# Kernel tuning notes

Hardware: AMD Instinct MI355X
Metric: run time of the kernel (lower is better)

The kernel has to match this reference:

```python
import jax, jax.numpy as jnp
import numpy as np

TOP_K = 30
NUM_RBF = 16
MAXREL = 32


def _normalize(x, eps=1e-12):
    return x / jnp.maximum(jnp.linalg.norm(x, axis=-1, keepdims=True), eps)


def gather_edges(edges, idx):
    # edges [B,L,L,C], idx [B,L,K] -> [B,L,K,C]
    return jnp.take_along_axis(edges, idx[..., None], axis=2)


def gather_nodes(nodes, idx):
    # nodes [B,L,C], idx [B,L,K] -> [B,L,K,C]
    B, L, K = idx.shape
    flat = idx.reshape(B, L * K)
    g = jnp.take_along_axis(nodes, flat[:, :, None], axis=1)
    return g.reshape(B, L, K, nodes.shape[-1])


def _rbf(D):
    mu = jnp.linspace(2.0, 22.0, NUM_RBF)
    sigma = (22.0 - 2.0) / NUM_RBF
    return jnp.exp(-(((D[..., None] - mu) / sigma) ** 2))


def _get_rbf(A, B, E_idx):
    D = jnp.sqrt(jnp.sum((A[:, :, None, :] - B[:, None, :, :]) ** 2, -1) + 1e-6)
    Dn = gather_edges(D[..., None], E_idx)[..., 0]
    return _rbf(Dn)


def _dist(X, mask, eps=1e-6):
    mask2 = mask[:, None, :] * mask[:, :, None]
    dX = X[:, None, :, :] - X[:, :, None, :]
    D = mask2 * jnp.sqrt(jnp.sum(dX ** 2, -1) + eps)
    D_max = jnp.max(D, -1, keepdims=True)
    D_adjust = D + (1.0 - mask2) * D_max
    k = min(TOP_K, X.shape[1])
    neg_vals, E_idx = jax.lax.top_k(-D_adjust, k)  # smallest-k distances
    D_neighbors = -neg_vals
    mask_neighbors = gather_edges(mask2[..., None], E_idx)
    return D_neighbors, E_idx, mask_neighbors


def _quaternions(R):
    # R [B,L,K,3,3] -> Q [B,L,K,4]
    diag = jnp.diagonal(R, axis1=-2, axis2=-1)
    Rxx, Ryy, Rzz = diag[..., 0], diag[..., 1], diag[..., 2]
    magnitudes = 0.5 * jnp.sqrt(jnp.abs(1.0 + jnp.stack(
        [Rxx - Ryy - Rzz, -Rxx + Ryy - Rzz, -Rxx - Ryy + Rzz], -1)))
    signs = jnp.sign(jnp.stack([
        R[..., 2, 1] - R[..., 1, 2],
        R[..., 0, 2] - R[..., 2, 0],
        R[..., 1, 0] - R[..., 0, 1]], -1))
    xyz = signs * magnitudes
    w = jnp.sqrt(jax.nn.relu(1.0 + jnp.sum(diag, -1, keepdims=True))) / 2.0
    Q = jnp.concatenate((xyz, w), -1)
    return _normalize(Q)


def _orientations_coarse(X, E_idx, eps=1e-6):
    dX = X[:, 1:, :] - X[:, :-1, :]
    dX_norm = jnp.linalg.norm(dX, axis=-1)
    dX_mask = ((dX_norm > 3.6) & (dX_norm < 4.0)).astype(X.dtype)
    dX = dX * dX_mask[:, :, None]
    U = _normalize(dX)
    u_2, u_1, u_0 = U[:, :-2, :], U[:, 1:-1, :], U[:, 2:, :]
    n_2 = _normalize(jnp.cross(u_2, u_1))
    n_1 = _normalize(jnp.cross(u_1, u_0))
    cosA = jnp.clip(-(u_1 * u_0).sum(-1), -1 + eps, 1 - eps)
    A = jnp.arccos(cosA)
    cosD = jnp.clip((n_2 * n_1).sum(-1), -1 + eps, 1 - eps)
    Dang = jnp.sign((u_2 * n_1).sum(-1)) * jnp.arccos(cosD)
    AD = jnp.stack((jnp.cos(A), jnp.sin(A) * jnp.cos(Dang),
                    jnp.sin(A) * jnp.sin(Dang)), -1)
    AD = jnp.pad(AD, ((0, 0), (1, 2), (0, 0)))  # [B,L,3]
    o_1 = _normalize(u_2 - u_1)
    O = jnp.stack((o_1, n_2, jnp.cross(o_1, n_2)), -2)  # [B,L-3,3,3]
    O = O.reshape(O.shape[0], O.shape[1], 9)
    O = jnp.pad(O, ((0, 0), (1, 2), (0, 0)))  # [B,L,9]
    O_nb = gather_nodes(O, E_idx).reshape(E_idx.shape[0], E_idx.shape[1], E_idx.shape[2], 3, 3)
    X_nb = gather_nodes(X, E_idx)
    Om = O.reshape(O.shape[0], O.shape[1], 3, 3)
    dXn = X_nb - X[:, :, None, :]
    dU = _normalize(jnp.einsum('blij,blkj->blki', Om, dXn))
    R = jnp.einsum('blji,blkjm->blkim', Om, O_nb)  # O^T @ O_neighbors
    Q = _quaternions(R)
    return AD, jnp.concatenate((dU, Q), -1)  # [B,L,3], [B,L,K,7]


def _forward(Ca, mask, residue_idx, chain_labels, pos_W, pos_b, edge_W, ln_g, ln_b):
    D_neighbors, E_idx, mask_neighbors = _dist(Ca, mask)
    Ca_0 = jnp.pad(Ca[:, :-1, :], ((0, 0), (1, 0), (0, 0)))
    Ca_1 = Ca
    Ca_2 = jnp.pad(Ca[:, 1:, :], ((0, 0), (0, 1), (0, 0)))
    V, O_features = _orientations_coarse(Ca, E_idx)
    RBF_all = jnp.concatenate([
        _rbf(D_neighbors),
        _get_rbf(Ca_0, Ca_0, E_idx),
        _get_rbf(Ca_2, Ca_2, E_idx),
        _get_rbf(Ca_0, Ca_1, E_idx),
        _get_rbf(Ca_0, Ca_2, E_idx),
        _get_rbf(Ca_1, Ca_0, E_idx),
        _get_rbf(Ca_1, Ca_2, E_idx),
        _get_rbf(Ca_2, Ca_0, E_idx),
        _get_rbf(Ca_2, Ca_1, E_idx)], -1)  # [B,L,K,144]
    offset = residue_idx[:, :, None] - residue_idx[:, None, :]
    offset = gather_edges(offset[..., None], E_idx)[..., 0]
    d_chains = (chain_labels[:, :, None] - chain_labels[:, None, :] == 0).astype(jnp.int32)
    E_chains = gather_edges(d_chains[..., None], E_idx)[..., 0]
    d = jnp.clip(offset + MAXREL, 0, 2 * MAXREL) * E_chains + (1 - E_chains) * (2 * MAXREL + 1)
    d_onehot = jax.nn.one_hot(d, 2 * MAXREL + 2, dtype=pos_W.dtype)
    E_positional = d_onehot @ pos_W + pos_b
    E = jnp.concatenate((E_positional, RBF_all, O_features), -1)  # [B,L,K,167]
    E = E @ edge_W  # no bias
    mu = jnp.mean(E, -1, keepdims=True)
    var = jnp.var(E, -1, keepdims=True)
    E = (E - mu) / jnp.sqrt(var + 1e-5) * ln_g + ln_b
    return E, E_idx


def setup_inputs() -> dict:
    key = jax.random.key(0)
    k1, k2, k3 = jax.random.split(key, 3)
    B, L = 2, 4096
    Ca = jax.random.normal(k1, (B, L, 3), dtype=jnp.float32) * 10.0
    mask = jnp.ones((B, L), dtype=jnp.float32)
    residue_idx = jnp.arange(B * L, dtype=jnp.int32).reshape(B, L) % L
    chain_labels = jnp.zeros((B, L), dtype=jnp.int32)
    pos_W = jax.random.normal(k2, (2 * MAXREL + 2, 16), dtype=jnp.float32) * 0.1
    pos_b = jnp.zeros((16,), dtype=jnp.float32)
    edge_in = 16 + NUM_RBF * 9 + 7  # 167
    edge_W = jax.random.normal(k3, (edge_in, 128), dtype=jnp.float32) * 0.05
    ln_g = jnp.ones((128,), dtype=jnp.float32)
    ln_b = jnp.zeros((128,), dtype=jnp.float32)
    return {"Ca": Ca, "mask": mask, "residue_idx": residue_idx,
            "chain_labels": chain_labels, "pos_W": pos_W, "pos_b": pos_b,
            "edge_W": edge_W, "ln_g": ln_g, "ln_b": ln_b}


def reference(Ca, mask, residue_idx, chain_labels, pos_W, pos_b, edge_W, ln_g, ln_b):
    return _forward(Ca, mask, residue_idx, chain_labels, pos_W, pos_b, edge_W, ln_g, ln_b)
```

## Files before the change

kernel.cpp:

```cpp
#include <hip/hip_runtime.h>
#include <math.h>

constexpr int Lc   = 4096;
constexpr int Bc   = 2;
constexpr int KNB  = 30;
constexpr int NF   = 167;
constexpr int NC   = 128;
constexpr int KP   = 200;
constexpr int NKT  = 6;
constexpr int CAP  = 512;

typedef __attribute__((ext_vector_type(8))) short bf16x8;
typedef __attribute__((ext_vector_type(4))) float f32x4;

struct V3 { float x, y, z; };

__device__ __forceinline__ float sgnf(float v) {
    return (v > 0.f) ? 1.f : ((v < 0.f) ? -1.f : 0.f);
}
__device__ __forceinline__ unsigned long long umin64(unsigned long long a, unsigned long long b) {
    return a < b ? a : b;
}
__device__ __forceinline__ void splitbf(float v, unsigned short& h, unsigned short& l) {
    unsigned u = __float_as_uint(v);
    h = (unsigned short)(u >> 16);
    float fh = __uint_as_float((unsigned)h << 16);
    l = (unsigned short)(__float_as_uint(v - fh) >> 16);
}
__device__ __forceinline__ unsigned cvtpk(float a, float b) {
    unsigned r;
    asm("v_cvt_pk_bf16_f32 %0, %1, %2" : "=v"(r) : "v"(a), "v"(b));
    return r;
}

__device__ __forceinline__ V3 unit_seg(float dx, float dy, float dz) {
    float n = sqrtf(dx * dx + dy * dy + dz * dz);
    float m = (n > 3.6f && n < 4.0f) ? 1.f : 0.f;
    float nn = fmaxf(m * n, 1e-12f);
    V3 r; r.x = dx * m / nn; r.y = dy * m / nn; r.z = dz * m / nn;
    return r;
}

__global__ __launch_bounds__(256) void topk_prep_kernel(
    const float* __restrict__ Ca, const float* __restrict__ mask,
    float* __restrict__ EidxF, int* __restrict__ EidxI,
    float* __restrict__ O, const float* __restrict__ W,
    unsigned short* __restrict__ Wh, unsigned short* __restrict__ Wl,
    int rows) {
    const int t = threadIdx.x;

    if (blockIdx.x >= rows) {
        int pb = blockIdx.x - rows;
        if (pb < 32) {
            int idx = pb * 256 + t;
            if (idx >= Bc * Lc) return;
            int b = idx >> 12, l = idx & (Lc - 1);
            float* o = O + (size_t)idx * 9;
            if (l < 1 || l >= Lc - 2) {
#pragma unroll
                for (int q = 0; q < 9; ++q) o[q] = 0.f;
                return;
            }
            const float* C = Ca + ((size_t)b * Lc + (l - 1)) * 3;
            V3 u2 = unit_seg(C[3] - C[0], C[4] - C[1], C[5] - C[2]);
            V3 u1 = unit_seg(C[6] - C[3], C[7] - C[4], C[8] - C[5]);
            float nx = u2.y * u1.z - u2.z * u1.y;
            float ny = u2.z * u1.x - u2.x * u1.z;
            float nz = u2.x * u1.y - u2.y * u1.x;
            float nn = fmaxf(sqrtf(nx * nx + ny * ny + nz * nz), 1e-12f);
            nx /= nn; ny /= nn; nz /= nn;
            float ox = u2.x - u1.x, oy = u2.y - u1.y, oz = u2.z - u1.z;
            float on = fmaxf(sqrtf(ox * ox + oy * oy + oz * oz), 1e-12f);
            ox /= on; oy /= on; oz /= on;
            o[0] = ox; o[1] = oy; o[2] = oz;
            o[3] = nx; o[4] = ny; o[5] = nz;
            o[6] = oy * nz - oz * ny;
            o[7] = oz * nx - ox * nz;
            o[8] = ox * ny - oy * nx;
        } else {
            int tt = (pb - 32) * 256 + t;
            if (tt >= NKT * 8 * 64) return;
            int lane = tt & 63, nt = (tt >> 6) & 7, kt = tt >> 9;
            int n = nt * 16 + (lane & 15);
            int kbase = kt * 32 + (lane >> 4) * 8;
            __align__(16) unsigned short h[8], l[8];
#pragma unroll
            for (int j = 0; j < 8; ++j) {
                int k = kbase + j;
                float v = (k < NF) ? W[(size_t)k * NC + n] : 0.f;
                splitbf(v, h[j], l[j]);
            }
            size_t o = (size_t)tt * 8;
            *(bf16x8*)(Wh + o) = *(const bf16x8*)h;
            *(bf16x8*)(Wl + o) = *(const bf16x8*)l;
        }
        return;
    }

    const int row = blockIdx.x;
    const int b = row >> 12, i = row & (Lc - 1);
    const float* CaB = Ca + (size_t)b * Lc * 3;
    const float* mB  = mask + (size_t)b * Lc;
    const float xi = CaB[i * 3 + 0], yi = CaB[i * 3 + 1], zi = CaB[i * 3 + 2];
    const float mi = mB[i];

    __shared__ unsigned long long cand[CAP];
    __shared__ float redf[4];
    __shared__ int redi[2][4];
    __shared__ int candN;

    const int lane = t & 63, wid = t >> 6;
    if (t == 0) candN = 0;

    const int j0 = t * 16;
    const float4* Ca4 = (const float4*)(CaB + (size_t)j0 * 3);
    const float4* M4  = (const float4*)(mB + j0);

    float ss[16], m2a[16];
    float lmax = -1e30f;
#pragma unroll
    for (int u = 0; u < 4; ++u) {
        float4 c0 = Ca4[u * 3 + 0];
        float4 c1 = Ca4[u * 3 + 1];
        float4 c2 = Ca4[u * 3 + 2];
        float4 mm = M4[u];
        float px[4] = {c0.x, c0.w, c1.z, c2.y};
        float py[4] = {c0.y, c1.x, c1.w, c2.z};
        float pz[4] = {c0.z, c1.y, c2.x, c2.w};
        float pm[4] = {mm.x, mm.y, mm.z, mm.w};
#pragma unroll
        for (int q = 0; q < 4; ++q) {
            float dx = px[q] - xi, dy = py[q] - yi, dz = pz[q] - zi;
            float s = dx * dx + dy * dy + dz * dz;
            float m2 = mi * pm[q];
            float v = m2 * s;
            ss[u * 4 + q] = v; m2a[u * 4 + q] = m2;
            lmax = fmaxf(lmax, v);
        }
    }
    for (int off = 32; off; off >>= 1) lmax = fmaxf(lmax, __shfl_xor(lmax, off));
    if (lane == 0) redf[wid] = lmax;
    __syncthreads();
    const float ssmax = fmaxf(fmaxf(redf[0], redf[1]), fmaxf(redf[2], redf[3]));

#pragma unroll
    for (int k = 0; k < 16; ++k) ss[k] = ss[k] + (1.f - m2a[k]) * ssmax;

    float T = ssmax * 0.037772f;
    int c = 0;
    for (int iter = 0; iter < 32; ++iter) {
        int lc = 0;
#pragma unroll
        for (int k = 0; k < 16; ++k) lc += (ss[k] <= T) ? 1 : 0;
        for (int off = 32; off; off >>= 1) lc += __shfl_xor(lc, off);
        if (lane == 0) redi[iter & 1][wid] = lc;
        __syncthreads();
        c = redi[iter & 1][0] + redi[iter & 1][1] + redi[iter & 1][2] + redi[iter & 1][3];
        if (c >= KNB && c <= 64) break;
        if (iter >= 12 && c >= KNB && c <= CAP) break;
        if (c < KNB) {
            if (c == 0) T *= 2.89f;
            else {
                float f = cbrtf((float)(KNB + 15) / (float)c);
                T *= fminf(2.89f, 1.1025f * f * f);
            }
        } else {
            float f = cbrtf(45.f / (float)c);
            T *= fmaxf(0.3025f, 1.1025f * f * f);
        }
    }

#pragma unroll
    for (int k = 0; k < 16; ++k) {
        if (ss[k] <= T) {
            int idx = atomicAdd(&candN, 1);
            if (idx < CAP)
                cand[idx] = ((unsigned long long)__float_as_uint(ss[k]) << 32) |
                            (unsigned)(j0 + k);
        }
    }
    __syncthreads();

    if (wid == 0) {
        int C = candN; if (C > CAP) C = CAP;
        if (C <= 64) {
            unsigned long long key = (lane < C) ? cand[lane] : ~0ULL;
#pragma unroll
            for (int size = 2; size <= 64; size <<= 1) {
#pragma unroll
                for (int stride = size >> 1; stride; stride >>= 1) {
                    unsigned long long other = __shfl_xor(key, stride);
                    bool dirUp = ((lane & size) == 0);
                    bool takeMin = ((lane & stride) == 0) ? dirUp : !dirUp;
                    bool less = other < key;
                    unsigned long long mn = less ? other : key;
                    unsigned long long mx = less ? key : other;
                    key = takeMin ? mn : mx;
                }
            }
            if (lane < KNB) {
                int jw = (int)(key & 0xFFFFFFFFULL);
                EidxF[(size_t)row * KNB + lane] = (float)jw;
                EidxI[(size_t)row * KNB + lane] = jw;
            }
        } else {
            unsigned long long r[CAP / 64];
#pragma unroll
            for (int q = 0; q < CAP / 64; ++q) {
                int idx = lane + q * 64;
                r[q] = (idx < C) ? cand[idx] : ~0ULL;
            }
            for (int p = 0; p < KNB; ++p) {
                unsigned long long mn = r[0];
#pragma unroll
                for (int q = 1; q < CAP / 64; ++q) mn = umin64(mn, r[q]);
                for (int off = 32; off; off >>= 1) mn = umin64(mn, __shfl_xor(mn, off));
                if (lane == 0) {
                    int jw = (int)(mn & 0xFFFFFFFFULL);
                    EidxF[(size_t)row * KNB + p] = (float)jw;
                    EidxI[(size_t)row * KNB + p] = jw;
                }
#pragma unroll
                for (int q = 0; q < CAP / 64; ++q) if (r[q] == mn) r[q] = ~0ULL;
            }
        }
    }
}

__global__ __launch_bounds__(256) void edge_kernel(
    const float* __restrict__ Ca, const int* __restrict__ ridx,
    const int* __restrict__ clab, const float* __restrict__ pos_W,
    const float* __restrict__ pos_b,
    const unsigned short* __restrict__ Wh, const unsigned short* __restrict__ Wl,
    const float* __restrict__ ln_g, const float* __restrict__ ln_b,
    const int* __restrict__ EidxI, const float* __restrict__ Omat,
    float* __restrict__ outE) {
    const int row = blockIdx.x;
    const int b = row >> 12, i = row & (Lc - 1);
    const int tid = threadIdx.x, lane = tid & 63, w = tid >> 6;

    __shared__ __align__(16) unsigned short Fh[32][KP];
    __shared__ float Ssum[32][4];
    __shared__ float Ssq[32][4];
    __shared__ float2 Mstat[32];
    __shared__ int Ej[32];

    const float* CaB = Ca + (size_t)b * Lc * 3;

    for (int q = tid; q < 32 * 33; q += 256) {
        int r = q / 33, c = 167 + q % 33;
        Fh[r][c] = 0;
    }
    for (int q = tid; q < 2 * 167; q += 256) {
        int r = 30 + q / 167, c = q % 167;
        Fh[r][c] = 0;
    }
    if (tid < KNB) Ej[tid] = EidxI[(size_t)row * KNB + tid];
    __syncthreads();

    auto putF2 = [&](int e, int k, float va, float vb) {
        *(unsigned*)&Fh[e][k] = cvtpk(va, vb);
    };
    auto loadC = [&](int n) {
        V3 r;
        if (n >= 0 && n < Lc) { r.x = CaB[n*3]; r.y = CaB[n*3+1]; r.z = CaB[n*3+2]; }
        else { r.x = 0.f; r.y = 0.f; r.z = 0.f; }
        return r;
    };

    auto rbf_task = [&](int r) {
        int e = r % 30, g = r / 30 + 1;
        int j = Ej[e];
        int pa = (int)((0xA5084u >> (2 * g)) & 3u);
        int pb = (int)((0x48984u >> (2 * g)) & 3u);
        V3 A = loadC(i - 1 + pa);
        V3 B = loadC(j - 1 + pb);
        float dx = A.x - B.x, dy = A.y - B.y, dz = A.z - B.z;
        float D8 = sqrtf(dx * dx + dy * dy + dz * dz + 1e-6f) * (1.f / 1.25f);
        int k0 = 16 * g;
#pragma unroll
        for (int m = 0; m < 16; m += 2) {
            float z0 = D8 - (2.f + (20.f / 15.f) * (float)m) * (1.f / 1.25f);
            float z1 = D8 - (2.f + (20.f / 15.f) * (float)(m + 1)) * (1.f / 1.25f);
            putF2(e, k0 + m, __expf(-z0 * z0), __expf(-z1 * z1));
        }
    };

    rbf_task(tid);

    if (w == 0) {
        if (lane < 14) rbf_task(256 + lane);
    } else if (w == 1) {
        if (lane < KNB) {
            int e = lane, j = Ej[e];
            int off = ridx[(size_t)b * Lc + i] - ridx[(size_t)b * Lc + j];
            int ec = (clab[(size_t)b * Lc + i] == clab[(size_t)b * Lc + j]) ? 1 : 0;
            int d = ec ? min(max(off + 32, 0), 64) : 65;
#pragma unroll
            for (int cc = 0; cc < 16; cc += 2)
                putF2(e, cc, pos_W[d * 16 + cc] + pos_b[cc],
                             pos_W[d * 16 + cc + 1] + pos_b[cc + 1]);
        }
    } else if (w == 2) {
        if (lane < KNB) {
            int e = lane, j = Ej[e];
            const float* Om = Omat + (size_t)row * 9;
            const float* On = Omat + ((size_t)b * Lc + j) * 9;
            V3 Ai = loadC(i), Bj = loadC(j);
            float dvx = Bj.x - Ai.x, dvy = Bj.y - Ai.y, dvz = Bj.z - Ai.z;
            float u0 = Om[0] * dvx + Om[1] * dvy + Om[2] * dvz;
            float u1 = Om[3] * dvx + Om[4] * dvy + Om[5] * dvz;
            float u2 = Om[6] * dvx + Om[7] * dvy + Om[8] * dvz;
            float un = fmaxf(sqrtf(u0 * u0 + u1 * u1 + u2 * u2), 1e-12f);
            float R[3][3];
#pragma unroll
            for (int a = 0; a < 3; ++a)
#pragma unroll
                for (int m = 0; m < 3; ++m)
                    R[a][m] = Om[0 * 3 + a] * On[0 * 3 + m] +
                              Om[1 * 3 + a] * On[1 * 3 + m] +
                              Om[2 * 3 + a] * On[2 * 3 + m];
            float Rxx = R[0][0], Ryy = R[1][1], Rzz = R[2][2];
            float m0 = 0.5f * sqrtf(fabsf(1.f + Rxx - Ryy - Rzz));
            float m1 = 0.5f * sqrtf(fabsf(1.f - Rxx + Ryy - Rzz));
            float m2 = 0.5f * sqrtf(fabsf(1.f - Rxx - Ryy + Rzz));
            float qx = sgnf(R[2][1] - R[1][2]) * m0;
            float qy = sgnf(R[0][2] - R[2][0]) * m1;
            float qz = sgnf(R[1][0] - R[0][1]) * m2;
            float qw = sqrtf(fmaxf(0.f, 1.f + Rxx + Ryy + Rzz)) * 0.5f;
            float qn = fmaxf(sqrtf(qx * qx + qy * qy + qz * qz + qw * qw), 1e-12f);
            putF2(e, 160, u0 / un, u1 / un);
            putF2(e, 162, u2 / un, qx / qn);
            putF2(e, 164, qy / qn, qz / qn);
            putF2(e, 166, qw / qn, 0.f);
        }
    }
    __syncthreads();

    const int arow = lane & 15, agrp = lane >> 4;
    const int ng0 = w * 2;
    f32x4 acc[2][2];
#pragma unroll
    for (int m = 0; m < 2; ++m)
#pragma unroll
        for (int n = 0; n < 2; ++n) acc[m][n] = (f32x4){0.f, 0.f, 0.f, 0.f};

    const bf16x8* WhF = (const bf16x8*)Wh;
    const bf16x8* WlF = (const bf16x8*)Wl;

#pragma unroll
    for (int kt = 0; kt < NKT; ++kt) {
        const int kof = kt * 32 + agrp * 8;
        bf16x8 a0 = *(const bf16x8*)&Fh[arow][kof];
        bf16x8 a1 = *(const bf16x8*)&Fh[16 + arow][kof];
        bf16x8 b0h = WhF[(kt * 8 + ng0) * 64 + lane];
        bf16x8 b1h = WhF[(kt * 8 + ng0 + 1) * 64 + lane];
        bf16x8 b0l = WlF[(kt * 8 + ng0) * 64 + lane];
        bf16x8 b1l = WlF[(kt * 8 + ng0 + 1) * 64 + lane];

        acc[0][0] = __builtin_amdgcn_mfma_f32_16x16x32_bf16(a0, b0h, acc[0][0], 0, 0, 0);
        acc[0][0] = __builtin_amdgcn_mfma_f32_16x16x32_bf16(a0, b0l, acc[0][0], 0, 0, 0);
        acc[0][1] = __builtin_amdgcn_mfma_f32_16x16x32_bf16(a0, b1h, acc[0][1], 0, 0, 0);
        acc[0][1] = __builtin_amdgcn_mfma_f32_16x16x32_bf16(a0, b1l, acc[0][1], 0, 0, 0);
        acc[1][0] = __builtin_amdgcn_mfma_f32_16x16x32_bf16(a1, b0h, acc[1][0], 0, 0, 0);
        acc[1][0] = __builtin_amdgcn_mfma_f32_16x16x32_bf16(a1, b0l, acc[1][0], 0, 0, 0);
        acc[1][1] = __builtin_amdgcn_mfma_f32_16x16x32_bf16(a1, b1h, acc[1][1], 0, 0, 0);
        acc[1][1] = __builtin_amdgcn_mfma_f32_16x16x32_bf16(a1, b1l, acc[1][1], 0, 0, 0);
    }

    float ps[2][4], pq[2][4];
#pragma unroll
    for (int m = 0; m < 2; ++m)
#pragma unroll
        for (int r = 0; r < 4; ++r) {
            float v0 = acc[m][0][r], v1 = acc[m][1][r];
            ps[m][r] = v0 + v1;
            pq[m][r] = v0 * v0 + v1 * v1;
        }
#pragma unroll
    for (int off = 1; off < 16; off <<= 1) {
#pragma unroll
        for (int m = 0; m < 2; ++m)
#pragma unroll
            for (int r = 0; r < 4; ++r) {
                ps[m][r] += __shfl_xor(ps[m][r], off);
                pq[m][r] += __shfl_xor(pq[m][r], off);
            }
    }
    if (arow == 0) {
#pragma unroll
        for (int m = 0; m < 2; ++m)
#pragma unroll
            for (int r = 0; r < 4; ++r) {
                int me = m * 16 + agrp * 4 + r;
                Ssum[me][w] = ps[m][r];
                Ssq[me][w] = pq[m][r];
            }
    }
    __syncthreads();
    if (tid < 32) {
        float s = Ssum[tid][0] + Ssum[tid][1] + Ssum[tid][2] + Ssum[tid][3];
        float q = Ssq[tid][0] + Ssq[tid][1] + Ssq[tid][2] + Ssq[tid][3];
        float mean = s * (1.f / 128.f);
        float var = q * (1.f / 128.f) - mean * mean;
        Mstat[tid] = make_float2(mean, 1.f / sqrtf(var + 1e-5f));
    }
    __syncthreads();

    float gg[2], bb[2];
#pragma unroll
    for (int n = 0; n < 2; ++n) {
        int ce = (ng0 + n) * 16 + arow;
        gg[n] = ln_g[ce];
        bb[n] = ln_b[ce];
    }
#pragma unroll
    for (int m = 0; m < 2; ++m)
#pragma unroll
        for (int r = 0; r < 4; ++r) {
            int me = m * 16 + agrp * 4 + r;
            if (me >= KNB) continue;
            float2 st = Mstat[me];
            size_t base = ((size_t)row * KNB + me) * NC;
#pragma unroll
            for (int n = 0; n < 2; ++n) {
                int ce = (ng0 + n) * 16 + arow;
                outE[base + ce] = (acc[m][n][r] - st.x) * st.y * gg[n] + bb[n];
            }
        }
}

extern "C" void kernel_launch(void* const* d_in, const int* in_sizes, int n_in,
                              void* d_out, int out_size, void* d_ws, size_t ws_size,
                              hipStream_t stream) {
    const float* Ca     = (const float*)d_in[0];
    const float* mask   = (const float*)d_in[1];
    const int*   ridx   = (const int*)d_in[2];
    const int*   clab   = (const int*)d_in[3];
    const float* pos_W  = (const float*)d_in[4];
    const float* pos_b  = (const float*)d_in[5];
    const float* edge_W = (const float*)d_in[6];
    const float* ln_g   = (const float*)d_in[7];
    const float* ln_b   = (const float*)d_in[8];

    float* outE  = (float*)d_out;
    float* EidxF = outE + (size_t)Bc * Lc * KNB * NC;

    float* Omat  = (float*)d_ws;
    int*   EidxI = (int*)(Omat + (size_t)Bc * Lc * 9);
    unsigned short* Wh = (unsigned short*)(EidxI + (size_t)Bc * Lc * KNB);
    unsigned short* Wl = Wh + (size_t)NKT * 8 * 64 * 8;

    const int rows = Bc * Lc;
    topk_prep_kernel<<<rows + 44, 256, 0, stream>>>(Ca, mask, EidxF, EidxI,
                                                    Omat, edge_W, Wh, Wl, rows);
    edge_kernel<<<rows, 256, 0, stream>>>(Ca, ridx, clab, pos_W, pos_b, Wh, Wl,
                                          ln_g, ln_b, EidxI, Omat, outE);
}
```

Baseline: 131.4 us.

## Probe four thresholds in one reduction and switch to strided coordinate loads

The first threshold-search step now counts candidates against four geometrically spaced thresholds in a single pass and reduction, then picks the smallest threshold that yields at least K candidates. This is meant to cut the number of block-wide reduction and barrier rounds in the iterative top-k threshold search. Coordinate loading also changes from each thread reading 16 contiguous points with float4 to a strided pattern (t + k*256) using scalar loads. The strided pattern coalesces better across threads but gives up the vector loads. Candidate indices are updated to match.

```diff
diff --git a/kernel.cpp b/kernel.cpp
--- a/kernel.cpp
+++ b/kernel.cpp
@@ -107,36 +107,25 @@
     __shared__ unsigned long long cand[CAP];
     __shared__ float redf[4];
     __shared__ int redi[2][4];
+    __shared__ int redi4[4][4];
     __shared__ int candN;
 
     const int lane = t & 63, wid = t >> 6;
     if (t == 0) candN = 0;
 
-    const int j0 = t * 16;
-    const float4* Ca4 = (const float4*)(CaB + (size_t)j0 * 3);
-    const float4* M4  = (const float4*)(mB + j0);
-
     float ss[16], m2a[16];
     float lmax = -1e30f;
 #pragma unroll
-    for (int u = 0; u < 4; ++u) {
-        float4 c0 = Ca4[u * 3 + 0];
-        float4 c1 = Ca4[u * 3 + 1];
-        float4 c2 = Ca4[u * 3 + 2];
-        float4 mm = M4[u];
-        float px[4] = {c0.x, c0.w, c1.z, c2.y};
-        float py[4] = {c0.y, c1.x, c1.w, c2.z};
-        float pz[4] = {c0.z, c1.y, c2.x, c2.w};
-        float pm[4] = {mm.x, mm.y, mm.z, mm.w};
-#pragma unroll
-        for (int q = 0; q < 4; ++q) {
-            float dx = px[q] - xi, dy = py[q] - yi, dz = pz[q] - zi;
-            float s = dx * dx + dy * dy + dz * dz;
-            float m2 = mi * pm[q];
-            float v = m2 * s;
-            ss[u * 4 + q] = v; m2a[u * 4 + q] = m2;
-            lmax = fmaxf(lmax, v);
-        }
+    for (int k = 0; k < 16; ++k) {
+        int j = t + k * 256;
+        float dx = CaB[j * 3 + 0] - xi;
+        float dy = CaB[j * 3 + 1] - yi;
+        float dz = CaB[j * 3 + 2] - zi;
+        float s = dx * dx + dy * dy + dz * dz;
+        float m2 = mi * mB[j];
+        float v = m2 * s;
+        ss[k] = v; m2a[k] = m2;
+        lmax = fmaxf(lmax, v);
     }
     for (int off = 32; off; off >>= 1) lmax = fmaxf(lmax, __shfl_xor(lmax, off));
     if (lane == 0) redf[wid] = lmax;
@@ -146,16 +135,40 @@
 #pragma unroll
     for (int k = 0; k < 16; ++k) ss[k] = ss[k] + (1.f - m2a[k]) * ssmax;
 
-    float T = ssmax * 0.037772f;
-    int c = 0;
-    for (int iter = 0; iter < 32; ++iter) {
-        int lc = 0;
-#pragma unroll
-        for (int k = 0; k < 16; ++k) lc += (ss[k] <= T) ? 1 : 0;
-        for (int off = 32; off; off >>= 1) lc += __shfl_xor(lc, off);
-        if (lane == 0) redi[iter & 1][wid] = lc;
+    const float Tb = ssmax * 0.037772f;
+    float T;
+    int c;
+    {
+        const float t0 = Tb, t1 = Tb * 3.f, t2 = Tb * 9.f, t3 = Tb * 27.f;
+        int l0 = 0, l1 = 0, l2 = 0, l3 = 0;
+#pragma unroll
+        for (int k = 0; k < 16; ++k) {
+            float v = ss[k];
+            l0 += (v <= t0) ? 1 : 0;
+            l1 += (v <= t1) ? 1 : 0;
+            l2 += (v <= t2) ? 1 : 0;
+            l3 += (v <= t3) ? 1 : 0;
+        }
+        for (int off = 32; off; off >>= 1) {
+            l0 += __shfl_xor(l0, off); l1 += __shfl_xor(l1, off);
+            l2 += __shfl_xor(l2, off); l3 += __shfl_xor(l3, off);
+        }
+        if (lane == 0) {
+            redi4[wid][0] = l0; redi4[wid][1] = l1;
+            redi4[wid][2] = l2; redi4[wid][3] = l3;
+        }
         __syncthreads();
-        c = redi[iter & 1][0] + redi[iter & 1][1] + redi[iter & 1][2] + redi[iter & 1][3];
+        int c0 = redi4[0][0] + redi4[1][0] + redi4[2][0] + redi4[3][0];
+        int c1 = redi4[0][1] + redi4[1][1] + redi4[2][1] + redi4[3][1];
+        int c2 = redi4[0][2] + redi4[1][2] + redi4[2][2] + redi4[3][2];
+        int c3 = redi4[0][3] + redi4[1][3] + redi4[2][3] + redi4[3][3];
+        if (c0 >= KNB)      { T = t0; c = c0; }
+        else if (c1 >= KNB) { T = t1; c = c1; }
+        else if (c2 >= KNB) { T = t2; c = c2; }
+        else                { T = t3; c = c3; }
+    }
+
+    for (int iter = 1; iter < 32; ++iter) {
         if (c >= KNB && c <= 64) break;
         if (iter >= 12 && c >= KNB && c <= CAP) break;
         if (c < KNB) {
@@ -168,6 +181,13 @@
             float f = cbrtf(45.f / (float)c);
             T *= fmaxf(0.3025f, 1.1025f * f * f);
         }
+        int lc = 0;
+#pragma unroll
+        for (int k = 0; k < 16; ++k) lc += (ss[k] <= T) ? 1 : 0;
+        for (int off = 32; off; off >>= 1) lc += __shfl_xor(lc, off);
+        if (lane == 0) redi[iter & 1][wid] = lc;
+        __syncthreads();
+        c = redi[iter & 1][0] + redi[iter & 1][1] + redi[iter & 1][2] + redi[iter & 1][3];
     }
 
 #pragma unroll
@@ -176,7 +196,7 @@
             int idx = atomicAdd(&candN, 1);
             if (idx < CAP)
                 cand[idx] = ((unsigned long long)__float_as_uint(ss[k]) << 32) |
-                            (unsigned)(j0 + k);
+                            (unsigned)(t + k * 256);
         }
     }
     __syncthreads();
```

Measured after the change: 116.8 us, median of 2. -11.1%, faster.
